# Kernel tuning notes

Measured on AMD Instinct MI355X. Metric: run time of the kernel, lower is better.

Reference implementation:

```python
import jax, jax.numpy as jnp
import numpy as np

N = 50000
E = 800000
IN, HID, OUT, HEADS = 128, 64, 64, 3
NEG_SLOPE = 0.2
BN_EPS = 1e-5


def setup_inputs() -> dict:
    key = jax.random.key(0)
    ks = jax.random.split(key, 20)
    s = 0.05
    inp = {
        "x": jax.random.normal(ks[0], (N, IN), jnp.float32),
        "edge_index": jax.random.randint(ks[1], (2, E), 0, N, jnp.int32),
        # layer 0: in=128 -> heads=3, C=64 (concat -> 192)
        "Wl0": jax.random.normal(ks[2], (IN, HEADS * HID), jnp.float32) * s,
        "bl0": jnp.zeros((HEADS * HID,), jnp.float32),
        "Wr0": jax.random.normal(ks[3], (IN, HEADS * HID), jnp.float32) * s,
        "br0": jnp.zeros((HEADS * HID,), jnp.float32),
        "att0": jax.random.normal(ks[4], (HEADS, HID), jnp.float32) * s,
        "bias0": jnp.zeros((HEADS * HID,), jnp.float32),
        "gamma0": jnp.ones((HEADS * HID,), jnp.float32),
        "beta0": jnp.zeros((HEADS * HID,), jnp.float32),
        # layer 1: in=192 -> heads=1, C=64
        "Wl1": jax.random.normal(ks[5], (HEADS * HID, OUT), jnp.float32) * s,
        "bl1": jnp.zeros((OUT,), jnp.float32),
        "Wr1": jax.random.normal(ks[6], (HEADS * HID, OUT), jnp.float32) * s,
        "br1": jnp.zeros((OUT,), jnp.float32),
        "att1": jax.random.normal(ks[7], (1, OUT), jnp.float32) * s,
        "bias1": jnp.zeros((OUT,), jnp.float32),
        "gamma1": jnp.ones((OUT,), jnp.float32),
        "beta1": jnp.zeros((OUT,), jnp.float32),
    }
    return inp


def _gatv2_layer(x, Wl, bl, Wr, br, att, bias, src, dst, n):
    H, C = att.shape
    xl = (x @ Wl + bl).reshape(n, H, C)
    xr = (x @ Wr + br).reshape(n, H, C)
    e = jax.nn.leaky_relu(xl[src] + xr[dst], NEG_SLOPE)      # [E,H,C]
    logit = jnp.einsum("ehc,hc->eh", e, att)                 # [E,H]
    m = jax.lax.stop_gradient(jax.ops.segment_max(logit, dst, num_segments=n))
    p = jnp.exp(logit - m[dst])
    denom = jax.ops.segment_sum(p, dst, num_segments=n)
    alpha = p / denom[dst]                                   # per-dst softmax
    out = jax.ops.segment_sum(alpha[:, :, None] * xl[src], dst, num_segments=n)
    return out.reshape(n, H * C) + bias


def _bn(x, gamma, beta):
    mu = x.mean(0)
    var = x.var(0)
    return (x - mu) * jax.lax.rsqrt(var + BN_EPS) * gamma + beta


def reference(x, edge_index, Wl0, bl0, Wr0, br0, att0, bias0, gamma0, beta0,
              Wl1, bl1, Wr1, br1, att1, bias1, gamma1, beta1):
    n = x.shape[0]
    loops = jnp.arange(n, dtype=edge_index.dtype)
    src = jnp.concatenate([edge_index[0], loops])  # PyG add_self_loops=True
    dst = jnp.concatenate([edge_index[1], loops])
    h = _gatv2_layer(x, Wl0, bl0, Wr0, br0, att0, bias0, src, dst, n)
    h = _bn(jax.nn.relu(h), gamma0, beta0)
    h = _gatv2_layer(h, Wl1, bl1, Wr1, br1, att1, bias1, src, dst, n)
    h = _bn(jax.nn.relu(h), gamma1, beta1)
    return h
```

## Files before the change

kernel.cpp:

```cpp
#include <hip/hip_runtime.h>
#include <hip/hip_bf16.h>

#define LRELU_SLOPE 0.2f
#define BN_EPS 1e-5f

typedef __attribute__((ext_vector_type(8))) short short8v;
typedef __attribute__((ext_vector_type(4))) float float4v;

static __device__ __forceinline__ unsigned short f2bf(float f) {
    __hip_bfloat16 b = __float2bfloat16(f);
    return *reinterpret_cast<unsigned short*>(&b);
}
static __device__ __forceinline__ void unpack2(unsigned int u, float& f0, float& f1) {
    f0 = __uint_as_float(u << 16);
    f1 = __uint_as_float(u & 0xffff0000u);
}
static __device__ __forceinline__ float lrelu(float x) {
    return fmaxf(x, LRELU_SLOPE * x);
}

__global__ void convcount_kernel(const float* __restrict__ Wl0, const float* __restrict__ Wr0,
                                 const float* __restrict__ Wl1, const float* __restrict__ Wr1,
                                 unsigned short* __restrict__ Wt0, unsigned short* __restrict__ Wt1,
                                 const int* __restrict__ dst, int* __restrict__ counts, int E) {
    int idx = blockIdx.x * blockDim.x + threadIdx.x;
    if (idx < 384 * 128) {
        int c = idx >> 7, k = idx & 127;
        float v = (c < 192) ? Wl0[(size_t)k * 192 + c] : Wr0[(size_t)k * 192 + (c - 192)];
        Wt0[idx] = f2bf(v);
    } else if (idx < 384 * 128 + 128 * 192) {
        int i2 = idx - 384 * 128;
        int c = i2 / 192, k = i2 % 192;
        float v = (c < 64) ? Wl1[(size_t)k * 64 + c] : Wr1[(size_t)k * 64 + (c - 64)];
        Wt1[i2] = f2bf(v);
    }
    if (idx < E) atomicAdd(&counts[dst[idx]], 1);
}

__global__ void scanA_kernel(const int* __restrict__ counts, int* __restrict__ offs,
                             int* __restrict__ blkSum, int n) {
    __shared__ int wsum[4];
    const int lane = threadIdx.x & 63;
    const int wv = threadIdx.x >> 6;
    int i0 = blockIdx.x * 1024 + (int)threadIdx.x * 4;
    int v0 = (i0 + 0 < n) ? counts[i0 + 0] : 0;
    int v1 = (i0 + 1 < n) ? counts[i0 + 1] : 0;
    int v2 = (i0 + 2 < n) ? counts[i0 + 2] : 0;
    int v3 = (i0 + 3 < n) ? counts[i0 + 3] : 0;
    int s4 = v0 + v1 + v2 + v3;
    int s = s4;
    #pragma unroll
    for (int off = 1; off < 64; off <<= 1) {
        int t = __shfl_up(s, off, 64);
        if (lane >= off) s += t;
    }
    if (lane == 63) wsum[wv] = s;
    __syncthreads();
    int wpre = 0;
    for (int w = 0; w < wv; ++w) wpre += wsum[w];
    int excl = wpre + s - s4;
    if (i0 + 0 < n) offs[i0 + 0] = excl;
    excl += v0;
    if (i0 + 1 < n) offs[i0 + 1] = excl;
    excl += v1;
    if (i0 + 2 < n) offs[i0 + 2] = excl;
    excl += v2;
    if (i0 + 3 < n) offs[i0 + 3] = excl;
    if (threadIdx.x == 255) blkSum[blockIdx.x] = wpre + s;
}

__global__ void scanC_kernel(int* __restrict__ offs, const int* __restrict__ blkSum, int n, int E) {
    __shared__ int baseSh;
    const int b = blockIdx.x;
    if (threadIdx.x < 64) {
        int acc = 0;
        for (int i = threadIdx.x; i < b; i += 64) acc += blkSum[i];
        #pragma unroll
        for (int off = 1; off < 64; off <<= 1) acc += __shfl_xor(acc, off, 64);
        if (threadIdx.x == 0) baseSh = acc;
    }
    __syncthreads();
    const int base = baseSh;
    int i = b * 1024 + (int)threadIdx.x * 4;
    if (i + 3 < n) {
        int4 v = *reinterpret_cast<int4*>(&offs[i]);
        v.x += base; v.y += base; v.z += base; v.w += base;
        *reinterpret_cast<int4*>(&offs[i]) = v;
    } else {
        #pragma unroll
        for (int k = 0; k < 4; ++k)
            if (i + k < n) offs[i + k] += base;
    }
    if (b == 0 && threadIdx.x == 0) offs[n] = E;
}

__global__ void scatter_kernel(const int* __restrict__ src, const int* __restrict__ dst,
                               const int* __restrict__ offs, int* __restrict__ cursor,
                               int* __restrict__ esrc, int E) {
    int e = blockIdx.x * blockDim.x + threadIdx.x;
    if (e < E) {
        int d = dst[e];
        int pos = offs[d] + atomicAdd(&cursor[d], 1);
        esrc[pos] = src[e];
    }
}

template <int K, int NCH, bool BN>
__global__ __launch_bounds__(256) void mfma_dual_gemm(
    const float* __restrict__ X,
    const unsigned short* __restrict__ Wt,
    const float* __restrict__ bl, const float* __restrict__ br,
    const float* __restrict__ stats, const float* __restrict__ gamma,
    const float* __restrict__ beta, float invN,
    unsigned short* __restrict__ xlB, unsigned short* __restrict__ xrB, int N) {
    constexpr int LDA = 40;
    const int rowBase = blockIdx.x * 128;
    const int colBase = blockIdx.y * 128;

    __shared__ unsigned short XS[128 * LDA];
    __shared__ unsigned short WS[128 * LDA];
    __shared__ float ssA[K], ssB[K];

    const int tid = threadIdx.x;
    const int lane = tid & 63;
    const int wv = tid >> 6;
    const int lrow = lane & 15;
    const int lk = lane >> 4;

    if (BN) {
        for (int c = tid; c < K; c += 256) {
            float mu = stats[c] * invN;
            float var = stats[K + c] * invN - mu * mu;
            float sc = gamma[c] * rsqrtf(var + BN_EPS);
            ssA[c] = sc;
            ssB[c] = beta[c] - mu * sc;
        }
        __syncthreads();
    }

    float4v acc[2][8];
    #pragma unroll
    for (int i = 0; i < 2; ++i)
        #pragma unroll
        for (int j = 0; j < 8; ++j) acc[i][j] = (float4v){0.f, 0.f, 0.f, 0.f};

    for (int k0 = 0; k0 < K; k0 += 32) {
        {
            int r = tid >> 3;
            int kq = (tid & 7) * 4;
            float4 sc0, sc1;
            if (BN) {
                sc0 = *reinterpret_cast<const float4*>(&ssA[k0 + kq]);
                sc1 = *reinterpret_cast<const float4*>(&ssB[k0 + kq]);
            }
            #pragma unroll
            for (int i = 0; i < 4; ++i) {
                int row = r + 32 * i;
                int gr = rowBase + row;
                float4 v = make_float4(0.f, 0.f, 0.f, 0.f);
                if (gr < N) v = *reinterpret_cast<const float4*>(&X[(size_t)gr * K + k0 + kq]);
                if (BN) {
                    v.x = v.x * sc0.x + sc1.x;
                    v.y = v.y * sc0.y + sc1.y;
                    v.z = v.z * sc0.z + sc1.z;
                    v.w = v.w * sc0.w + sc1.w;
                }
                ushort4 u;
                u.x = f2bf(v.x); u.y = f2bf(v.y); u.z = f2bf(v.z); u.w = f2bf(v.w);
                *reinterpret_cast<ushort4*>(&XS[row * LDA + kq]) = u;
            }
        }
        {
            int c = tid >> 2;
            int kq8 = (tid & 3) * 8;
            #pragma unroll
            for (int i = 0; i < 2; ++i) {
                int col = c + 64 * i;
                uint4 w = *reinterpret_cast<const uint4*>(&Wt[(size_t)(colBase + col) * K + k0 + kq8]);
                *reinterpret_cast<uint4*>(&WS[col * LDA + kq8]) = w;
            }
        }
        __syncthreads();
        short8v aF[2], bF[8];
        #pragma unroll
        for (int rb = 0; rb < 2; ++rb)
            aF[rb] = *reinterpret_cast<const short8v*>(&XS[(wv * 32 + rb * 16 + lrow) * LDA + lk * 8]);
        #pragma unroll
        for (int cb = 0; cb < 8; ++cb)
            bF[cb] = *reinterpret_cast<const short8v*>(&WS[(cb * 16 + lrow) * LDA + lk * 8]);
        #pragma unroll
        for (int rb = 0; rb < 2; ++rb)
            #pragma unroll
            for (int cb = 0; cb < 8; ++cb)
                acc[rb][cb] = __builtin_amdgcn_mfma_f32_16x16x32_bf16(aF[rb], bF[cb], acc[rb][cb], 0, 0, 0);
        __syncthreads();
    }
    #pragma unroll
    for (int cb = 0; cb < 8; ++cb) {
        int cgG = colBase + cb * 16 + lrow;
        bool isR = cgG >= NCH;
        int cc = isR ? cgG - NCH : cgG;
        int hh = cc >> 6;
        int ch = cc & 63;
        float bv = isR ? br[cc] : bl[cc];
        unsigned short* dstB = (isR ? xrB : xlB) + (size_t)hh * N * 64 + ch;
        #pragma unroll
        for (int rb = 0; rb < 2; ++rb) {
            #pragma unroll
            for (int r = 0; r < 4; ++r) {
                int row = rowBase + wv * 32 + rb * 16 + lk * 4 + r;
                if (row < N) dstB[(size_t)row * 64] = f2bf(acc[rb][cb][r] + bv);
            }
        }
    }
}

template <int H>
__global__ __launch_bounds__(256) void gat_agg_head_kernel(
    const unsigned short* __restrict__ xlB,
    const unsigned short* __restrict__ xrB,
    const int* __restrict__ offs, const int* __restrict__ esrc,
    const float* __restrict__ att,
    const float* __restrict__ bias,
    float* __restrict__ outh,
    int N) {
    const int h = blockIdx.y;
    const unsigned short* xl_ = xlB + (size_t)h * N * 64;
    const unsigned short* xr_ = xrB + (size_t)h * N * 64;
    const int lane = threadIdx.x & 63;
    const int node = blockIdx.x * 4 + (threadIdx.x >> 6);
    if (node >= N) return;
    const int j = lane >> 3;
    const int cg = (lane & 7) * 8;

    float xr[8], at[8], acc[8];
    float den = 0.f;
    {
        uint4 u = *reinterpret_cast<const uint4*>(&xr_[(size_t)node * 64 + cg]);
        unpack2(u.x, xr[0], xr[1]); unpack2(u.y, xr[2], xr[3]);
        unpack2(u.z, xr[4], xr[5]); unpack2(u.w, xr[6], xr[7]);
        float4 a0 = *reinterpret_cast<const float4*>(&att[h * 64 + cg]);
        float4 a1 = *reinterpret_cast<const float4*>(&att[h * 64 + cg + 4]);
        at[0] = a0.x; at[1] = a0.y; at[2] = a0.z; at[3] = a0.w;
        at[4] = a1.x; at[5] = a1.y; at[6] = a1.z; at[7] = a1.w;
        #pragma unroll
        for (int c = 0; c < 8; ++c) acc[c] = 0.f;
    }

    const int beg = offs[node];
    const int total = offs[node + 1] - beg + 1;

    uint4 u0, u1, u2, u3;
    {
        int c0 = (j      < total) ? j      : total - 1;
        int c1 = (j + 8  < total) ? j + 8  : total - 1;
        int c2 = (j + 16 < total) ? j + 16 : total - 1;
        int c3 = (j + 24 < total) ? j + 24 : total - 1;
        int s0 = (c0 == 0) ? node : esrc[beg + c0 - 1];
        int s1 = (c1 == 0) ? node : esrc[beg + c1 - 1];
        int s2 = (c2 == 0) ? node : esrc[beg + c2 - 1];
        int s3 = (c3 == 0) ? node : esrc[beg + c3 - 1];
        u0 = *reinterpret_cast<const uint4*>(&xl_[(size_t)s0 * 64 + cg]);
        u1 = *reinterpret_cast<const uint4*>(&xl_[(size_t)s1 * 64 + cg]);
        u2 = *reinterpret_cast<const uint4*>(&xl_[(size_t)s2 * 64 + cg]);
        u3 = *reinterpret_cast<const uint4*>(&xl_[(size_t)s3 * 64 + cg]);
    }
    for (int t = 0; t < total; t += 8) {
        float xlv[8];
        unpack2(u0.x, xlv[0], xlv[1]); unpack2(u0.y, xlv[2], xlv[3]);
        unpack2(u0.z, xlv[4], xlv[5]); unpack2(u0.w, xlv[6], xlv[7]);
        u0 = u1; u1 = u2; u2 = u3;
        const int v4 = t + 32 + j;
        if (v4 < total) {
            int s4 = esrc[beg + v4 - 1];
            u3 = *reinterpret_cast<const uint4*>(&xl_[(size_t)s4 * 64 + cg]);
        }
        float s = 0.f;
        #pragma unroll
        for (int c = 0; c < 8; ++c) s += lrelu(xlv[c] + xr[c]) * at[c];
        #pragma unroll
        for (int off = 1; off <= 4; off <<= 1) s += __shfl_xor(s, off, 64);
        const float w = (t + j < total) ? 1.f : 0.f;
        float p = w * __expf(s);
        den += p;
        #pragma unroll
        for (int c = 0; c < 8; ++c) acc[c] += p * xlv[c];
    }

    #pragma unroll
    for (int off = 8; off <= 32; off <<= 1) {
        den += __shfl_xor(den, off, 64);
        #pragma unroll
        for (int c = 0; c < 8; ++c) acc[c] += __shfl_xor(acc[c], off, 64);
    }

    if (j == 0) {
        float inv = 1.f / den;
        float4 b0 = *reinterpret_cast<const float4*>(&bias[h * 64 + cg]);
        float4 b1 = *reinterpret_cast<const float4*>(&bias[h * 64 + cg + 4]);
        float4 o0, o1;
        o0.x = fmaxf(acc[0] * inv + b0.x, 0.f); o0.y = fmaxf(acc[1] * inv + b0.y, 0.f);
        o0.z = fmaxf(acc[2] * inv + b0.z, 0.f); o0.w = fmaxf(acc[3] * inv + b0.w, 0.f);
        o1.x = fmaxf(acc[4] * inv + b1.x, 0.f); o1.y = fmaxf(acc[5] * inv + b1.y, 0.f);
        o1.z = fmaxf(acc[6] * inv + b1.z, 0.f); o1.w = fmaxf(acc[7] * inv + b1.w, 0.f);
        float* orow = &outh[(size_t)node * (H * 64) + h * 64 + cg];
        *reinterpret_cast<float4*>(orow) = o0;
        *reinterpret_cast<float4*>(orow + 4) = o1;
    }
}

template <int CH>
__global__ void bn_stats_kernel(const float* __restrict__ h, float* __restrict__ stats, int N) {
    const int c = threadIdx.x;
    float s = 0.f, q = 0.f;
    for (int r = blockIdx.x; r < N; r += gridDim.x) {
        float v = h[(size_t)r * CH + c];
        s += v;
        q += v * v;
    }
    atomicAdd(&stats[c], s);
    atomicAdd(&stats[CH + c], q);
}

__global__ void bn_finapply64_kernel(float* __restrict__ h, const float* __restrict__ stats,
                                     const float* __restrict__ gamma, const float* __restrict__ beta,
                                     float invN, size_t total4) {
    size_t i = (size_t)blockIdx.x * blockDim.x + threadIdx.x;
    if (i >= total4) return;
    size_t e = i * 4;
    int c = (int)(e & 63);
    float4 v = *reinterpret_cast<float4*>(&h[e]);
    #pragma unroll
    for (int k = 0; k < 4; ++k) {
        float mu = stats[c + k] * invN;
        float var = stats[64 + c + k] * invN - mu * mu;
        float sc = gamma[c + k] * rsqrtf(var + BN_EPS);
        (&v.x)[k] = ((&v.x)[k] - mu) * sc + beta[c + k];
    }
    *reinterpret_cast<float4*>(&h[e]) = v;
}

extern "C" void kernel_launch(void* const* d_in, const int* in_sizes, int n_in,
                              void* d_out, int out_size, void* d_ws, size_t ws_size,
                              hipStream_t stream) {
    const float* x     = (const float*)d_in[0];
    const int*   eidx  = (const int*)d_in[1];
    const float* Wl0   = (const float*)d_in[2];
    const float* bl0   = (const float*)d_in[3];
    const float* Wr0   = (const float*)d_in[4];
    const float* br0   = (const float*)d_in[5];
    const float* att0  = (const float*)d_in[6];
    const float* bias0 = (const float*)d_in[7];
    const float* g0    = (const float*)d_in[8];
    const float* be0   = (const float*)d_in[9];
    const float* Wl1   = (const float*)d_in[10];
    const float* bl1   = (const float*)d_in[11];
    const float* Wr1   = (const float*)d_in[12];
    const float* br1   = (const float*)d_in[13];
    const float* att1  = (const float*)d_in[14];
    const float* bias1 = (const float*)d_in[15];
    const float* g1    = (const float*)d_in[16];
    const float* be1   = (const float*)d_in[17];

    const int N = in_sizes[0] / 128;
    const int E = in_sizes[1] / 2;
    const int* srcIdx = eidx;
    const int* dstIdx = eidx + E;
    const int nChunks = (N + 1023) >> 10;
    const int nGroups = (N + 3) / 4;
    const float invN = 1.f / (float)N;

    char* base = (char*)d_ws;
    auto alloc = [&](size_t bytes) {
        char* p = base;
        base += (bytes + 255) & ~(size_t)255;
        return p;
    };
    unsigned short* projL = (unsigned short*)alloc((size_t)3 * N * 64 * 2);
    unsigned short* projR = (unsigned short*)alloc((size_t)3 * N * 64 * 2);
    float* h0    = (float*)alloc((size_t)N * 192 * 4);
    int*   offs  = (int*)alloc((size_t)(N + 1) * 4);
    int*   esrc  = (int*)alloc((size_t)E * 4);
    int*   blkSum= (int*)alloc((size_t)nChunks * 4);
    unsigned short* Wt0 = (unsigned short*)alloc((size_t)384 * 128 * 2);
    unsigned short* Wt1 = (unsigned short*)alloc((size_t)128 * 192 * 2);
    char* zeroBeg = base;
    int*   counts = (int*)alloc((size_t)N * 4);
    int*   cursor = (int*)alloc((size_t)N * 4);
    float* stats0 = (float*)alloc(384 * 4);
    float* stats1 = (float*)alloc(128 * 4);
    size_t zeroBytes = (size_t)(base - zeroBeg);

    hipMemsetAsync(zeroBeg, 0, zeroBytes, stream);

    {
        int work = E > (384 * 128 + 128 * 192) ? E : (384 * 128 + 128 * 192);
        convcount_kernel<<<(work + 255) / 256, 256, 0, stream>>>(Wl0, Wr0, Wl1, Wr1, Wt0, Wt1, dstIdx, counts, E);
    }
    scanA_kernel<<<nChunks, 256, 0, stream>>>(counts, offs, blkSum, N);
    scanC_kernel<<<nChunks, 256, 0, stream>>>(offs, blkSum, N, E);
    scatter_kernel<<<(E + 255) / 256, 256, 0, stream>>>(srcIdx, dstIdx, offs, cursor, esrc, E);

    {
        dim3 grid((N + 127) / 128, 3);
        mfma_dual_gemm<128, 192, false><<<grid, 256, 0, stream>>>(
            x, Wt0, bl0, br0, nullptr, nullptr, nullptr, 0.f, projL, projR, N);
    }
    {
        dim3 grid(nGroups, 3);
        gat_agg_head_kernel<3><<<grid, 256, 0, stream>>>(projL, projR, offs, esrc, att0, bias0, h0, N);
    }
    bn_stats_kernel<192><<<256, 192, 0, stream>>>(h0, stats0, N);

    {
        dim3 grid((N + 127) / 128, 1);
        mfma_dual_gemm<192, 64, true><<<grid, 256, 0, stream>>>(
            h0, Wt1, bl1, br1, stats0, g0, be0, invN, projL, projR, N);
    }
    float* out = (float*)d_out;
    {
        dim3 grid(nGroups, 1);
        gat_agg_head_kernel<1><<<grid, 256, 0, stream>>>(projL, projR, offs, esrc, att1, bias1, out, N);
    }
    bn_stats_kernel<64><<<256, 64, 0, stream>>>(out, stats1, N);
    {
        size_t tot4 = (size_t)N * 16;
        bn_finapply64_kernel<<<(unsigned)((tot4 + 255) / 256), 256, 0, stream>>>(out, stats1, g1, be1, invN, tot4);
    }
}
```

Measured before the change: 373.1 us.

## Remap head aggregation to 16 lanes per edge with DPP row reductions

The per-head GATv2 aggregation kernel now assigns 16 lanes × 4 channels per edge instead of 8 lanes × 8 channels, so each wave handles 4 edges per step instead of 8. The channel dot-product reduction uses DPP row rotations instead of xor shuffles, and the gather prefetch depth drops from 4 to 2 slots with 8-byte loads. The aim is to cut wasted lanes on low-degree nodes (average degree about 17) and to make the reduction cheaper. In exchange, the loop runs more iterations per node, loads are narrower, and fewer gathers are in flight to hide memory latency.

Result: slower. 396.7 us (+6.3%).

```diff
diff --git a/kernel.cpp b/kernel.cpp
--- a/kernel.cpp
+++ b/kernel.cpp
@@ -11,12 +11,16 @@
     __hip_bfloat16 b = __float2bfloat16(f);
     return *reinterpret_cast<unsigned short*>(&b);
 }
-static __device__ __forceinline__ void unpack2(unsigned int u, float& f0, float& f1) {
-    f0 = __uint_as_float(u << 16);
-    f1 = __uint_as_float(u & 0xffff0000u);
+static __device__ __forceinline__ float bf2f(unsigned short u) {
+    return __uint_as_float(((unsigned)u) << 16);
 }
 static __device__ __forceinline__ float lrelu(float x) {
     return fmaxf(x, LRELU_SLOPE * x);
+}
+template <int CTRL>
+static __device__ __forceinline__ float row_rot(float x) {
+    int t = __builtin_amdgcn_update_dpp(0, __float_as_int(x), CTRL, 0xF, 0xF, true);
+    return __int_as_float(t);
 }
 
 __global__ void convcount_kernel(const float* __restrict__ Wl0, const float* __restrict__ Wr0,
@@ -230,82 +234,71 @@
     const int lane = threadIdx.x & 63;
     const int node = blockIdx.x * 4 + (threadIdx.x >> 6);
     if (node >= N) return;
-    const int j = lane >> 3;
-    const int cg = (lane & 7) * 8;
-
-    float xr[8], at[8], acc[8];
+    const int j = lane >> 4;
+    const int cg = (lane & 15) * 4;
+
+    float xr4[4], at4[4], acc[4];
     float den = 0.f;
     {
-        uint4 u = *reinterpret_cast<const uint4*>(&xr_[(size_t)node * 64 + cg]);
-        unpack2(u.x, xr[0], xr[1]); unpack2(u.y, xr[2], xr[3]);
-        unpack2(u.z, xr[4], xr[5]); unpack2(u.w, xr[6], xr[7]);
-        float4 a0 = *reinterpret_cast<const float4*>(&att[h * 64 + cg]);
-        float4 a1 = *reinterpret_cast<const float4*>(&att[h * 64 + cg + 4]);
-        at[0] = a0.x; at[1] = a0.y; at[2] = a0.z; at[3] = a0.w;
-        at[4] = a1.x; at[5] = a1.y; at[6] = a1.z; at[7] = a1.w;
-        #pragma unroll
-        for (int c = 0; c < 8; ++c) acc[c] = 0.f;
+        ushort4 u = *reinterpret_cast<const ushort4*>(&xr_[(size_t)node * 64 + cg]);
+        xr4[0] = bf2f(u.x); xr4[1] = bf2f(u.y); xr4[2] = bf2f(u.z); xr4[3] = bf2f(u.w);
+        float4 a = *reinterpret_cast<const float4*>(&att[h * 64 + cg]);
+        at4[0] = a.x; at4[1] = a.y; at4[2] = a.z; at4[3] = a.w;
+        #pragma unroll
+        for (int c = 0; c < 4; ++c) acc[c] = 0.f;
     }
 
     const int beg = offs[node];
     const int total = offs[node + 1] - beg + 1;
-
-    uint4 u0, u1, u2, u3;
-    {
-        int c0 = (j      < total) ? j      : total - 1;
-        int c1 = (j + 8  < total) ? j + 8  : total - 1;
-        int c2 = (j + 16 < total) ? j + 16 : total - 1;
-        int c3 = (j + 24 < total) ? j + 24 : total - 1;
+    ushort4 u0, u1;
+    {
+        int c0 = (j < total) ? j : total - 1;
+        int c1 = (j + 4 < total) ? j + 4 : total - 1;
         int s0 = (c0 == 0) ? node : esrc[beg + c0 - 1];
         int s1 = (c1 == 0) ? node : esrc[beg + c1 - 1];
-        int s2 = (c2 == 0) ? node : esrc[beg + c2 - 1];
-        int s3 = (c3 == 0) ? node : esrc[beg + c3 - 1];
-        u0 = *reinterpret_cast<const uint4*>(&xl_[(size_t)s0 * 64 + cg]);
-        u1 = *reinterpret_cast<const uint4*>(&xl_[(size_t)s1 * 64 + cg]);
-        u2 = *reinterpret_cast<const uint4*>(&xl_[(size_t)s2 * 64 + cg]);
-        u3 = *reinterpret_cast<const uint4*>(&xl_[(size_t)s3 * 64 + cg]);
-    }
-    for (int t = 0; t < total; t += 8) {
-        float xlv[8];
-        unpack2(u0.x, xlv[0], xlv[1]); unpack2(u0.y, xlv[2], xlv[3]);
-        unpack2(u0.z, xlv[4], xlv[5]); unpack2(u0.w, xlv[6], xlv[7]);
-        u0 = u1; u1 = u2; u2 = u3;
-        const int v4 = t + 32 + j;
-        if (v4 < total) {
-            int s4 = esrc[beg + v4 - 1];
-            u3 = *reinterpret_cast<const uint4*>(&xl_[(size_t)s4 * 64 + cg]);
+        u0 = *reinterpret_cast<const ushort4*>(&xl_[(size_t)s0 * 64 + cg]);
+        u1 = *reinterpret_cast<const ushort4*>(&xl_[(size_t)s1 * 64 + cg]);
+    }
+    for (int t = 0; t < total; t += 4) {
+        float xl4[4];
+        xl4[0] = bf2f(u0.x); xl4[1] = bf2f(u0.y); xl4[2] = bf2f(u0.z); xl4[3] = bf2f(u0.w);
+        u0 = u1;
+        const int v2 = t + 8 + j;
+        if (v2 < total) {
+            int s2 = esrc[beg + v2 - 1];
+            u1 = *reinterpret_cast<const ushort4*>(&xl_[(size_t)s2 * 64 + cg]);
         }
-        float s = 0.f;
-        #pragma unroll
-        for (int c = 0; c < 8; ++c) s += lrelu(xlv[c] + xr[c]) * at[c];
-        #pragma unroll
-        for (int off = 1; off <= 4; off <<= 1) s += __shfl_xor(s, off, 64);
+        float s = lrelu(xl4[0] + xr4[0]) * at4[0];
+        s += lrelu(xl4[1] + xr4[1]) * at4[1];
+        s += lrelu(xl4[2] + xr4[2]) * at4[2];
+        s += lrelu(xl4[3] + xr4[3]) * at4[3];
+        s += row_rot<0x128>(s);
+        s += row_rot<0x124>(s);
+        s += row_rot<0x122>(s);
+        s += row_rot<0x121>(s);
         const float w = (t + j < total) ? 1.f : 0.f;
         float p = w * __expf(s);
         den += p;
         #pragma unroll
-        for (int c = 0; c < 8; ++c) acc[c] += p * xlv[c];
+        for (int c = 0; c < 4; ++c) acc[c] += p * xl4[c];
     }
 
     #pragma unroll
-    for (int off = 8; off <= 32; off <<= 1) {
+    for (int off = 16; off <= 32; off <<= 1) {
         den += __shfl_xor(den, off, 64);
         #pragma unroll
-        for (int c = 0; c < 8; ++c) acc[c] += __shfl_xor(acc[c], off, 64);
+        for (int c = 0; c < 4; ++c) acc[c] += __shfl_xor(acc[c], off, 64);
     }
 
     if (j == 0) {
         float inv = 1.f / den;
-        float4 b0 = *reinterpret_cast<const float4*>(&bias[h * 64 + cg]);
-        float4 b1 = *reinterpret_cast<const float4*>(&bias[h * 64 + cg + 4]);
-        float4 o0, o1;
-        o0.x = fmaxf(acc[0] * inv + b0.x, 0.f); o0.y = fmaxf(acc[1] * inv + b0.y, 0.f);
-        o0.z = fmaxf(acc[2] * inv + b0.z, 0.f); o0.w = fmaxf(acc[3] * inv + b0.w, 0.f);
-        o1.x = fmaxf(acc[4] * inv + b1.x, 0.f); o1.y = fmaxf(acc[5] * inv + b1.y, 0.f);
-        o1.z = fmaxf(acc[6] * inv + b1.z, 0.f); o1.w = fmaxf(acc[7] * inv + b1.w, 0.f);
-        float* orow = &outh[(size_t)node * (H * 64) + h * 64 + cg];
-        *reinterpret_cast<float4*>(orow) = o0;
-        *reinterpret_cast<float4*>(orow + 4) = o1;
+        float4 b4 = *reinterpret_cast<const float4*>(&bias[h * 64 + cg]);
+        float4 o;
+        o.x = fmaxf(acc[0] * inv + b4.x, 0.f);
+        o.y = fmaxf(acc[1] * inv + b4.y, 0.f);
+        o.z = fmaxf(acc[2] * inv + b4.z, 0.f);
+        o.w = fmaxf(acc[3] * inv + b4.w, 0.f);
+        *reinterpret_cast<float4*>(&outh[(size_t)node * (H * 64) + h * 64 + cg]) = o;
     }
 }
 
```
